# Optimization experiments

Hardware: AMD Instinct MI355X
Metric: run time of the kernel (lower is better)

The kernel has to match this reference:

```python
import jax, jax.numpy as jnp
import numpy as np

B, T, D, H = 2, 2048, 1024, 16
HD = D // H
FF = 4 * D
EPS = 1e-5


def rmsnorm(x, w):
    var = jnp.mean(jnp.square(x), axis=-1, keepdims=True)
    return x * jax.lax.rsqrt(var + EPS) * w


def setup_inputs() -> dict:
    key = jax.random.key(0)
    ks = jax.random.split(key, 17)
    sc = 0.02
    d = {}
    d["x"] = jax.random.normal(ks[0], (B, T, D), jnp.float32)
    d["x_token"] = jax.random.normal(ks[1], (B, T, D), jnp.float32)
    d["pos_emb"] = jax.random.normal(ks[2], (T, D), jnp.float32)
    d["lc_weight"] = jax.random.normal(ks[3], (1,), jnp.float32)
    d["Wq"] = jax.random.normal(ks[4], (D, D), jnp.float32) * sc  # per-head query weights stacked
    d["Wk"] = jax.random.normal(ks[5], (D, D), jnp.float32) * sc
    d["Wv"] = jax.random.normal(ks[6], (D, D), jnp.float32) * sc
    d["proj_w"] = jax.random.normal(ks[7], (D, D), jnp.float32) * sc
    d["proj_b"] = jnp.zeros((D,), jnp.float32)
    d["w1_w"] = jax.random.normal(ks[8], (FF, D), jnp.float32) * sc
    d["w1_b"] = jnp.zeros((FF,), jnp.float32)
    d["w2_w"] = jax.random.normal(ks[9], (D, FF), jnp.float32) * sc
    d["w2_b"] = jnp.zeros((D,), jnp.float32)
    d["w3_w"] = jax.random.normal(ks[10], (FF, D), jnp.float32) * sc
    d["w3_b"] = jnp.zeros((FF,), jnp.float32)
    d["norm1_w"] = jnp.ones((D,), jnp.float32)
    d["norm2_w"] = jnp.ones((D,), jnp.float32)
    return d


def reference(x, x_token, pos_emb, lc_weight, Wq, Wk, Wv, proj_w, proj_b,
              w1_w, w1_b, w2_w, w2_b, w3_w, w3_b, norm1_w, norm2_w):
    lc = jax.nn.sigmoid(lc_weight)  # scalar gate
    x_att = lc * x + (1.0 - lc) * x_token
    xn = rmsnorm(x_att, norm1_w)

    # q, v from normed gated input; k from raw positional embedding (faithful to source)
    q = (xn @ Wq.T).reshape(B, T, H, HD)
    k = (pos_emb @ Wk.T).reshape(T, H, HD)
    v = (xn @ Wv.T).reshape(B, T, H, HD)

    # NOTE: scale uses full model dim E (=D), not head_size, as in the source
    scores = jnp.einsum('bqhd,khd->bhqk', q, k) * (D ** -0.5)
    causal = jnp.tril(jnp.ones((T, T), bool))
    scores = jnp.where(causal, scores, -jnp.inf)
    p = jax.nn.softmax(scores, axis=-1)
    attn = jnp.einsum('bhqk,bkhd->bqhd', p, v).reshape(B, T, D)

    x = x + attn @ proj_w.T + proj_b

    xn2 = rmsnorm(x, norm2_w)
    h = jax.nn.silu(xn2 @ w1_w.T + w1_b) * (xn2 @ w3_w.T + w3_b)
    return x + h @ w2_w.T + w2_b
```

## Files before the change

### kernel.cpp

```cpp
#include <hip/hip_runtime.h>
#include <hip/hip_bf16.h>


typedef __hip_bfloat16 bf16;
typedef __attribute__((ext_vector_type(8))) short bf16x8;
typedef __attribute__((ext_vector_type(4))) float floatx4;

constexpr int cB = 2, cT = 2048, cD = 1024, cH = 16, cFF = 4096;
constexpr float cEPS = 1e-5f;
constexpr unsigned BF16_ONES = 0x3F803F80u;

__device__ __forceinline__ float b2f(bf16 x) { return __bfloat162float(x); }
__device__ __forceinline__ bf16  f2b(float x) { return __float2bfloat16(x); }
__device__ __forceinline__ unsigned short f2bu(float x) {
  bf16 t = __float2bfloat16(x);
  union { bf16 b; unsigned short u; } cv;
  cv.b = t;
  return cv.u;
}
__device__ __forceinline__ float loadR(const bf16* p)  { return b2f(*p); }
__device__ __forceinline__ float loadR(const float* p) { return *p; }

__device__ __forceinline__ void gload16(const bf16* g, unsigned short* l) {
  __builtin_amdgcn_global_load_lds(
      (const __attribute__((address_space(1))) void*)g,
      (__attribute__((address_space(3))) void*)l, 16, 0, 0);
}

__device__ __forceinline__ int xcd_remap1(int lin, int n) {
  return (lin & 7) * (n >> 3) + (lin >> 3);
}
__device__ __forceinline__ void xcd_remap(int& bx, int& by, int gx, int gy) {
  const int nwg = gx * gy;
  const int lin = by * gx + bx;
  const int nl  = xcd_remap1(lin, nwg);
  bx = nl % gx;
  by = nl / gx;
}

struct ConvArgs {
  const void* src[17];
  bf16* dst[17];
  int n[17];
  int sb[17];
};

__global__ __launch_bounds__(256) void convert_all_k(ConvArgs a) {
  const int bid = blockIdx.x;
  int seg = 0;
#pragma unroll
  for (int i = 1; i < 17; i++) seg = (bid >= a.sb[i]) ? i : seg;
  const int n = a.n[seg];
  const int i0 = (bid - a.sb[seg]) * 2048 + threadIdx.x * 8;
  if (i0 >= n) return;
  const bool isb = (((const unsigned*)a.src[15])[0] == BF16_ONES);
  const void* src = a.src[seg];
  bf16* dst = a.dst[seg];
  if (i0 + 8 <= n) {
    if (isb) {
      *(int4*)(dst + i0) = *(const int4*)((const bf16*)src + i0);
    } else {
      float4 f0 = *(const float4*)((const float*)src + i0);
      float4 f1 = *(const float4*)((const float*)src + i0 + 4);
      int4 ro;
      bf16* po = (bf16*)&ro;
      po[0] = f2b(f0.x); po[1] = f2b(f0.y); po[2] = f2b(f0.z); po[3] = f2b(f0.w);
      po[4] = f2b(f1.x); po[5] = f2b(f1.y); po[6] = f2b(f1.z); po[7] = f2b(f1.w);
      *(int4*)(dst + i0) = ro;
    }
  } else {
    for (int j = i0; j < n; j++)
      dst[j] = isb ? ((const bf16*)src)[j] : f2b(((const float*)src)[j]);
  }
}

template <int OUTK, typename ResT>
__device__ __forceinline__ void gemm_core64(
    const bf16* __restrict__ A, const bf16* __restrict__ W,
    const bf16* __restrict__ bias, const ResT* __restrict__ R,
    void* __restrict__ Cv,
    int N, int Kst, int kb, int klen, int m0, int n0,
    unsigned short* As, unsigned short* Bs)
{
  const int tid  = threadIdx.x;
  const int wave = tid >> 6;
  const int lane = tid & 63;
  const int l15  = lane & 15;
  const int quad = lane >> 4;
  const int wm   = (wave >> 1) * 64;
  const int wn   = (wave & 1) * 32;

  const int lr  = lane >> 2;
  const int lc8 = (lane & 3) * 8;
  const bf16* Ag0 = A + (size_t)(m0 + wave * 32 + lr) * Kst + kb + lc8;
  const bf16* Ag1 = Ag0 + (size_t)16 * Kst;
  const bf16* Bg0 = W + (size_t)(n0 + wave * 16 + lr) * Kst + kb + lc8;
  unsigned short* lA0 = &As[(wave * 32) * 32];
  unsigned short* lA1 = &As[(wave * 32 + 16) * 32];
  unsigned short* lB0 = &Bs[(wave * 16) * 32];

  floatx4 acc[4][2];
#pragma unroll
  for (int i = 0; i < 4; i++)
#pragma unroll
    for (int j = 0; j < 2; j++) acc[i][j] = (floatx4){0.f, 0.f, 0.f, 0.f};

  for (int k0 = 0; k0 < klen; k0 += 64) {
    gload16(Ag0 + k0, lA0);
    gload16(Ag1 + k0, lA1);
    gload16(Ag0 + k0 + 32, lA0 + 128 * 32);
    gload16(Ag1 + k0 + 32, lA1 + 128 * 32);
    gload16(Bg0 + k0, lB0);
    gload16(Bg0 + k0 + 32, lB0 + 64 * 32);
    __syncthreads();

    bf16x8 a[4][2], b[2][2];
#pragma unroll
    for (int t = 0; t < 4; t++)
#pragma unroll
      for (int kh = 0; kh < 2; kh++)
        a[t][kh] = *(const bf16x8*)&As[kh * 128 * 32 + (wm + t * 16 + l15) * 32 + quad * 8];
#pragma unroll
    for (int u = 0; u < 2; u++)
#pragma unroll
      for (int kh = 0; kh < 2; kh++)
        b[u][kh] = *(const bf16x8*)&Bs[kh * 64 * 32 + (wn + u * 16 + l15) * 32 + quad * 8];
#pragma unroll
    for (int tm = 0; tm < 4; tm++)
#pragma unroll
      for (int tn = 0; tn < 2; tn++)
#pragma unroll
        for (int kh = 0; kh < 2; kh++)
          acc[tm][tn] = __builtin_amdgcn_mfma_f32_16x16x32_bf16(a[tm][kh], b[tn][kh], acc[tm][tn], 0, 0, 0);
    __syncthreads();
  }

#pragma unroll
  for (int tm = 0; tm < 4; tm++) {
#pragma unroll
    for (int tn = 0; tn < 2; tn++) {
      const int row = m0 + wm + tm * 16 + quad * 4;
      const int col = n0 + wn + tn * 16 + l15;
      float bv = (OUTK != 3 && bias) ? b2f(bias[col]) : 0.f;
#pragma unroll
      for (int i = 0; i < 4; i++) {
        float val = acc[tm][tn][i] + bv;
        const size_t cidx = (size_t)(row + i) * N + col;
        if (OUTK == 3) {
          atomicAdd((float*)Cv + cidx, val);
        } else {
          if (R) val += loadR(&R[cidx]);
          if (OUTK == 0) ((bf16*)Cv)[cidx] = f2b(val);
          else           ((float*)Cv)[cidx] = val;
        }
      }
    }
  }
}

template <int OUTK, typename ResT>
__global__ __launch_bounds__(256) void gemm_f(
    const bf16* __restrict__ A, const bf16* __restrict__ W,
    const bf16* __restrict__ bias, const ResT* __restrict__ R,
    void* __restrict__ Cv, int N, int Kst, int kchunk, int gx, int gxy)
{
  __shared__ __align__(16) unsigned short As[2 * 128 * 32];
  __shared__ __align__(16) unsigned short Bs[2 * 64 * 32];
  const int lin = xcd_remap1(blockIdx.x, gridDim.x);
  const int kz  = lin / gxy;
  const int rem = lin % gxy;
  gemm_core64<OUTK, ResT>(A, W, bias, R, Cv, N, Kst, kz * kchunk, kchunk,
                          (rem / gx) * 128, (rem % gx) * 64, As, Bs);
}

__global__ __launch_bounds__(256) void gemm_qkv(
    const bf16* __restrict__ xn, const bf16* __restrict__ pos,
    const bf16* __restrict__ Wq, const bf16* __restrict__ Wv,
    const bf16* __restrict__ Wk,
    bf16* __restrict__ q, bf16* __restrict__ v, bf16* __restrict__ kb)
{
  __shared__ __align__(16) unsigned short As[2 * 128 * 32];
  __shared__ __align__(16) unsigned short Bs[2 * 64 * 32];
  const int lin = xcd_remap1(blockIdx.x, gridDim.x);
  int z, local;
  if (lin < 512)       { z = 0; local = lin; }
  else if (lin < 1024) { z = 1; local = lin - 512; }
  else                 { z = 2; local = lin - 1024; }
  const int gx = 16;
  const int by = local / gx, bx = local % gx;
  const bf16* A = (z == 2) ? pos : xn;
  const bf16* W = (z == 0) ? Wq : (z == 1) ? Wv : Wk;
  bf16* C = (z == 0) ? q : (z == 1) ? v : kb;
  gemm_core64<0, bf16>(A, W, nullptr, (const bf16*)nullptr, C,
                       cD, cD, 0, cD, by * 128, bx * 64, As, Bs);
}

__global__ __launch_bounds__(256) void gemm_w13(
    const bf16* __restrict__ A,
    const bf16* __restrict__ W1, const bf16* __restrict__ b1,
    const bf16* __restrict__ W3, const bf16* __restrict__ b3,
    bf16* __restrict__ H, int N, int K)
{
  __shared__ __align__(16) unsigned short As[2 * 128 * 32];
  __shared__ __align__(16) unsigned short B1s[2 * 64 * 32];
  __shared__ __align__(16) unsigned short B3s[2 * 64 * 32];
  const int lin = xcd_remap1(blockIdx.x, gridDim.x);
  const int by  = lin & 31;
  const int bx  = lin >> 5;
  const int m0  = by * 128;
  const int n0  = bx * 64;

  const int tid  = threadIdx.x;
  const int wave = tid >> 6;
  const int lane = tid & 63;
  const int l15  = lane & 15;
  const int quad = lane >> 4;
  const int wm   = (wave >> 1) * 64;
  const int wn   = (wave & 1) * 32;

  const int lr  = lane >> 2;
  const int lc8 = (lane & 3) * 8;
  const bf16* Ag0  = A  + (size_t)(m0 + wave * 32 + lr) * K + lc8;
  const bf16* Ag1  = Ag0 + (size_t)16 * K;
  const bf16* B1g0 = W1 + (size_t)(n0 + wave * 16 + lr) * K + lc8;
  const bf16* B3g0 = W3 + (size_t)(n0 + wave * 16 + lr) * K + lc8;
  unsigned short* lA0 = &As[(wave * 32) * 32];
  unsigned short* lA1 = &As[(wave * 32 + 16) * 32];
  unsigned short* l1B = &B1s[(wave * 16) * 32];
  unsigned short* l3B = &B3s[(wave * 16) * 32];

  floatx4 acc1[4][2], acc3[4][2];
#pragma unroll
  for (int i = 0; i < 4; i++)
#pragma unroll
    for (int j = 0; j < 2; j++) {
      acc1[i][j] = (floatx4){0.f, 0.f, 0.f, 0.f};
      acc3[i][j] = (floatx4){0.f, 0.f, 0.f, 0.f};
    }

  for (int k0 = 0; k0 < K; k0 += 64) {
    gload16(Ag0 + k0, lA0);
    gload16(Ag1 + k0, lA1);
    gload16(Ag0 + k0 + 32, lA0 + 128 * 32);
    gload16(Ag1 + k0 + 32, lA1 + 128 * 32);
    gload16(B1g0 + k0, l1B);
    gload16(B1g0 + k0 + 32, l1B + 64 * 32);
    gload16(B3g0 + k0, l3B);
    gload16(B3g0 + k0 + 32, l3B + 64 * 32);
    __syncthreads();

    bf16x8 a[4][2], v1[2][2], v3[2][2];
#pragma unroll
    for (int t = 0; t < 4; t++)
#pragma unroll
      for (int kh = 0; kh < 2; kh++)
        a[t][kh] = *(const bf16x8*)&As[kh * 128 * 32 + (wm + t * 16 + l15) * 32 + quad * 8];
#pragma unroll
    for (int u = 0; u < 2; u++)
#pragma unroll
      for (int kh = 0; kh < 2; kh++) {
        v1[u][kh] = *(const bf16x8*)&B1s[kh * 64 * 32 + (wn + u * 16 + l15) * 32 + quad * 8];
        v3[u][kh] = *(const bf16x8*)&B3s[kh * 64 * 32 + (wn + u * 16 + l15) * 32 + quad * 8];
      }
#pragma unroll
    for (int tm = 0; tm < 4; tm++)
#pragma unroll
      for (int tn = 0; tn < 2; tn++)
#pragma unroll
        for (int kh = 0; kh < 2; kh++) {
          acc1[tm][tn] = __builtin_amdgcn_mfma_f32_16x16x32_bf16(a[tm][kh], v1[tn][kh], acc1[tm][tn], 0, 0, 0);
          acc3[tm][tn] = __builtin_amdgcn_mfma_f32_16x16x32_bf16(a[tm][kh], v3[tn][kh], acc3[tm][tn], 0, 0, 0);
        }
    __syncthreads();
  }

#pragma unroll
  for (int tm = 0; tm < 4; tm++) {
#pragma unroll
    for (int tn = 0; tn < 2; tn++) {
      const int row = m0 + wm + tm * 16 + quad * 4;
      const int col = n0 + wn + tn * 16 + l15;
      const float bv1 = b2f(b1[col]);
      const float bv3 = b2f(b3[col]);
#pragma unroll
      for (int i = 0; i < 4; i++) {
        float g = acc1[tm][tn][i] + bv1;
        float u = acc3[tm][tn][i] + bv3;
        float val = g * (1.f / (1.f + __expf(-g))) * u;
        H[(size_t)(row + i) * N + col] = f2b(val);
      }
    }
  }
}

template <bool GATE, typename InT>
__global__ __launch_bounds__(256) void rmsnorm_k(
    const InT* __restrict__ X, const bf16* __restrict__ XT,
    const bf16* __restrict__ LC, const bf16* __restrict__ Wn,
    bf16* __restrict__ O, float* __restrict__ Z)
{
  const int row = blockIdx.x;
  const int tid = threadIdx.x;
  const size_t base = (size_t)row * cD;
  const int c = tid * 4;

  if (Z) *(float4*)(Z + base + c) = (float4){0.f, 0.f, 0.f, 0.f};

  float lc = 1.f, lc1 = 0.f;
  if (GATE) {
    float g = b2f(LC[0]);
    lc = 1.f / (1.f + __expf(-g));
    lc1 = 1.f - lc;
  }

  float xv[4];
  if (sizeof(InT) == 2) {
    ushort4 u = *(const ushort4*)((const unsigned short*)X + base + c);
    const bf16* pu = (const bf16*)&u;
#pragma unroll
    for (int i = 0; i < 4; i++) xv[i] = b2f(pu[i]);
  } else {
    float4 f = *(const float4*)((const float*)X + base + c);
    xv[0] = f.x; xv[1] = f.y; xv[2] = f.z; xv[3] = f.w;
  }
  if (GATE) {
    ushort4 u = *(const ushort4*)((const unsigned short*)XT + base + c);
    const bf16* pu = (const bf16*)&u;
#pragma unroll
    for (int i = 0; i < 4; i++) xv[i] = lc * xv[i] + lc1 * b2f(pu[i]);
  }

  float ss = xv[0] * xv[0] + xv[1] * xv[1] + xv[2] * xv[2] + xv[3] * xv[3];
#pragma unroll
  for (int off = 32; off; off >>= 1) ss += __shfl_xor(ss, off, 64);

  __shared__ float red[4];
  if ((tid & 63) == 0) red[tid >> 6] = ss;
  __syncthreads();
  float tot = red[0] + red[1] + red[2] + red[3];
  float rs = rsqrtf(tot * (1.f / cD) + cEPS);

  ushort4 o;
  bf16* po = (bf16*)&o;
#pragma unroll
  for (int i = 0; i < 4; i++) po[i] = f2b(xv[i] * rs * b2f(Wn[c + i]));
  *(ushort4*)((unsigned short*)O + base + c) = o;
}

__global__ __launch_bounds__(256) void combine_k(
    const float* __restrict__ P, const float* __restrict__ X2,
    const bf16* __restrict__ bias, void* __restrict__ out,
    const unsigned* __restrict__ dbits)
{
  const bool obf = (*dbits == BF16_ONES);
  const size_t idx = ((size_t)blockIdx.x * 256 + threadIdx.x) * 4;
  float4 p = *(const float4*)(P + idx);
  float4 x = *(const float4*)(X2 + idx);
  const int col = (int)(idx & (cD - 1));
  ushort4 bu = *(const ushort4*)((const unsigned short*)bias + col);
  const bf16* bb = (const bf16*)&bu;
  float v0 = p.x + x.x + b2f(bb[0]);
  float v1 = p.y + x.y + b2f(bb[1]);
  float v2 = p.z + x.z + b2f(bb[2]);
  float v3 = p.w + x.w + b2f(bb[3]);
  if (obf) {
    ushort4 o;
    bf16* po = (bf16*)&o;
    po[0] = f2b(v0); po[1] = f2b(v1); po[2] = f2b(v2); po[3] = f2b(v3);
    *(ushort4*)((unsigned short*)out + idx) = o;
  } else {
    *(float4*)((float*)out + idx) = (float4){v0, v1, v2, v3};
  }
}

__global__ __launch_bounds__(256) void fattn_k(
    const bf16* __restrict__ Q, const bf16* __restrict__ K,
    const bf16* __restrict__ V, bf16* __restrict__ O)
{
  constexpr int LQ = 72, LK = 72, LV = 72;
  __shared__ __align__(16) unsigned short Qs[64 * LQ];
  __shared__ __align__(16) unsigned short Ks[64 * LK];
  __shared__ __align__(16) unsigned short Vs[64 * LV];

  const int tid  = threadIdx.x;
  const int wave = tid >> 6;
  const int lane = tid & 63;
  const int l15  = lane & 15;
  const int quad = lane >> 4;
  const int blk  = blockIdx.x;
  const int qt   = 31 - (blk & 31);
  const int h    = (blk >> 5) & 15;
  const int b    = blk >> 9;
  const int q0   = qt * 64;

  const bf16* Qb = Q + ((size_t)b * cT) * cD + h * 64;
  const bf16* Kb = K + h * 64;
  const bf16* Vb = V + ((size_t)b * cT) * cD + h * 64;

  {
    const int qr = tid >> 2, qc = (tid & 3) * 16;
    const bf16* gq = Qb + (size_t)(q0 + qr) * cD + qc;
    *(int4*)&Qs[qr * LQ + qc]     = *(const int4*)(gq);
    *(int4*)&Qs[qr * LQ + qc + 8] = *(const int4*)(gq + 8);
  }
  __syncthreads();

  const int qw = wave * 16;
  bf16x8 qa[2];
#pragma unroll
  for (int dc = 0; dc < 2; dc++)
    qa[dc] = *(const bf16x8*)&Qs[(qw + l15) * LQ + dc * 32 + quad * 8];

  float l_p[4] = {0.f, 0.f, 0.f, 0.f};
  floatx4 oacc[4];
#pragma unroll
  for (int dt = 0; dt < 4; dt++) oacc[dt] = (floatx4){0.f, 0.f, 0.f, 0.f};

  const int ktiles = qt + 1;
  unsigned short* Pw = &Qs[qw * LQ];

  const int kr = tid >> 2, kc = (tid & 3) * 16;
  int4 kpre0, kpre1;
  unsigned short vpre[16];
  {
    const bf16* g = Kb + (size_t)kr * cD + kc;
    kpre0 = *(const int4*)g;
    kpre1 = *(const int4*)(g + 8);
    const unsigned short* gv = (const unsigned short*)(Vb + (size_t)(wave * 16) * cD + lane);
#pragma unroll
    for (int j = 0; j < 16; j++) vpre[j] = gv[(size_t)j * cD];
  }

  for (int it = 0; it < ktiles; ++it) {
    const int k0 = it * 64;
    __syncthreads();
    *(int4*)&Ks[kr * LK + kc]     = kpre0;
    *(int4*)&Ks[kr * LK + kc + 8] = kpre1;
    {
      union { unsigned short us[8]; int4 v4; } pk0, pk1;
#pragma unroll
      for (int j = 0; j < 8; j++) { pk0.us[j] = vpre[j]; pk1.us[j] = vpre[8 + j]; }
      *(int4*)&Vs[lane * LV + wave * 16]     = pk0.v4;
      *(int4*)&Vs[lane * LV + wave * 16 + 8] = pk1.v4;
    }
    __syncthreads();

    if (it + 1 < ktiles) {
      const bf16* g = Kb + (size_t)(k0 + 64 + kr) * cD + kc;
      kpre0 = *(const int4*)g;
      kpre1 = *(const int4*)(g + 8);
      const unsigned short* gv = (const unsigned short*)(Vb + (size_t)(k0 + 64 + wave * 16) * cD + lane);
#pragma unroll
      for (int j = 0; j < 16; j++) vpre[j] = gv[(size_t)j * cD];
    }

    floatx4 s[4];
#pragma unroll
    for (int st = 0; st < 4; st++) {
      bf16x8 kb0 = *(const bf16x8*)&Ks[(st * 16 + l15) * LK + quad * 8];
      bf16x8 kb1 = *(const bf16x8*)&Ks[(st * 16 + l15) * LK + 32 + quad * 8];
      s[st] = (floatx4){0.f, 0.f, 0.f, 0.f};
      s[st] = __builtin_amdgcn_mfma_f32_16x16x32_bf16(qa[0], kb0, s[st], 0, 0, 0);
      s[st] = __builtin_amdgcn_mfma_f32_16x16x32_bf16(qa[1], kb1, s[st], 0, 0, 0);
    }
    float p[4][4];
#pragma unroll
    for (int i = 0; i < 4; i++) {
      const int qrow = q0 + qw + quad * 4 + i;
#pragma unroll
      for (int st = 0; st < 4; st++) {
        const int kp = k0 + st * 16 + l15;
        float pv = (kp > qrow) ? 0.f : __expf(s[st][i] * 0.03125f);
        p[st][i] = pv;
        l_p[i] += pv;
      }
    }
#pragma unroll
    for (int st = 0; st < 4; st++)
#pragma unroll
      for (int i = 0; i < 4; i++)
        Pw[(quad * 4 + i) * LQ + st * 16 + l15] = f2bu(p[st][i]);
    bf16x8 pa[2];
#pragma unroll
    for (int pc = 0; pc < 2; pc++)
      pa[pc] = *(const bf16x8*)&Pw[l15 * LQ + pc * 32 + quad * 8];
#pragma unroll
    for (int dt = 0; dt < 4; dt++) {
      bf16x8 vb0 = *(const bf16x8*)&Vs[(dt * 16 + l15) * LV + quad * 8];
      bf16x8 vb1 = *(const bf16x8*)&Vs[(dt * 16 + l15) * LV + 32 + quad * 8];
      oacc[dt] = __builtin_amdgcn_mfma_f32_16x16x32_bf16(pa[0], vb0, oacc[dt], 0, 0, 0);
      oacc[dt] = __builtin_amdgcn_mfma_f32_16x16x32_bf16(pa[1], vb1, oacc[dt], 0, 0, 0);
    }
  }

  float rl[4];
#pragma unroll
  for (int i = 0; i < 4; i++) {
    float li = l_p[i];
#pragma unroll
    for (int off = 1; off < 16; off <<= 1) li += __shfl_xor(li, off, 64);
    rl[i] = 1.f / li;
  }
  const size_t obase = ((size_t)b * cT + q0 + qw) * cD + h * 64;
#pragma unroll
  for (int dt = 0; dt < 4; dt++)
#pragma unroll
    for (int i = 0; i < 4; i++)
      O[obase + (size_t)(quad * 4 + i) * cD + dt * 16 + l15] = f2b(oacc[dt][i] * rl[i]);
}

extern "C" void kernel_launch(void* const* d_in, const int* in_sizes, int n_in,
                              void* d_out, int out_size, void* d_ws, size_t ws_size,
                              hipStream_t stream) {
  char* ws = (char*)d_ws;
  const size_t MB = 1u << 20;
  const int BT = cB * cT;

  bf16* cxt  = (bf16*)(ws + 0);
  bf16* cpos = (bf16*)(ws + 8 * MB);
  bf16* q    = (bf16*)(ws + 12 * MB);
  bf16* kbuf = (bf16*)(ws + 20 * MB);
  bf16* v    = (bf16*)(ws + 24 * MB);
  bf16* h    = (bf16*)(ws + 0);
  size_t off = 32 * MB;
  auto alloc = [&](size_t bytes) -> char* {
    char* p = ws + off;
    off = (off + bytes + 255) & ~(size_t)255;
    return p;
  };
  bf16*  cx  = (bf16*)alloc((size_t)BT * cD * 2);
  bf16*  xn  = (bf16*)alloc((size_t)BT * cD * 2);
  float* x2  = (float*)alloc((size_t)BT * cD * 4);
  bf16*  xn2 = (bf16*)alloc((size_t)BT * cD * 2);
  float* part = (float*)(ws + 32 * MB);
  bf16* cin[17];
  cin[0] = cx; cin[1] = cxt; cin[2] = cpos;
  for (int i = 3; i < 17; i++) cin[i] = (bf16*)alloc((size_t)in_sizes[i] * 2);

  const unsigned* dbits = (const unsigned*)d_in[15];
  dim3 blk(256);

  ConvArgs ca;
  int nblk = 0;
  for (int i = 0; i < 17; i++) {
    ca.src[i] = d_in[i];
    ca.dst[i] = cin[i];
    ca.n[i] = in_sizes[i];
    ca.sb[i] = nblk;
    nblk += (in_sizes[i] + 2047) / 2048;
  }
  convert_all_k<<<nblk, blk, 0, stream>>>(ca);

  const bf16 *clc = cin[3], *cWq = cin[4], *cWk = cin[5], *cWv = cin[6];
  const bf16 *cprojw = cin[7], *cprojb = cin[8];
  const bf16 *cw1w = cin[9], *cw1b = cin[10], *cw2w = cin[11], *cw2b = cin[12];
  const bf16 *cw3w = cin[13], *cw3b = cin[14], *cn1 = cin[15], *cn2 = cin[16];

  rmsnorm_k<true, bf16><<<BT, blk, 0, stream>>>(cx, cxt, clc, cn1, xn, nullptr);
  gemm_qkv<<<1280, blk, 0, stream>>>(xn, cpos, cWq, cWv, cWk, q, v, kbuf);
  bf16* attn = xn;
  fattn_k<<<cB * cH * (cT / 64), blk, 0, stream>>>(q, kbuf, v, attn);
  gemm_f<1, bf16><<<512, blk, 0, stream>>>(
      attn, cprojw, cprojb, cx, x2, cD, cD, cD, 16, 512);
  rmsnorm_k<false, float><<<BT, blk, 0, stream>>>(
      x2, (const bf16*)nullptr, (const bf16*)nullptr, cn2, xn2, part);
  gemm_w13<<<2048, blk, 0, stream>>>(
      xn2, cw1w, cw1b, cw3w, cw3b, h, cFF, cD);
  gemm_f<3, float><<<1024, blk, 0, stream>>>(
      h, cw2w, nullptr, (const float*)nullptr, part, cD, cFF, 2048, 16, 512);
  combine_k<<<BT, blk, 0, stream>>>(part, x2, cw2b, d_out, dbits);
  (void)n_in; (void)out_size; (void)ws_size;
}
```

Before: 471.3 us.

## Double-buffer LDS tiles in GEMM kernels to overlap global loads with MFMA

Adds a second LDS buffer to the shared GEMM core and the fused W1/W3 GEMM. The next K-tile's global-to-LDS loads are issued right after the barrier, while MFMAs run on the current tile. This hides load latency behind compute and removes one barrier per K iteration. In exchange, LDS per block doubles (64KB for the W1/W3 kernel), which can lower how many blocks fit on a CU. The change also deletes an unused remap helper.

Measured after the change: 486.2 us. +3.2%, slower.

```diff
diff --git a/kernel.cpp b/kernel.cpp
--- a/kernel.cpp
+++ b/kernel.cpp
@@ -29,13 +29,6 @@
 
 __device__ __forceinline__ int xcd_remap1(int lin, int n) {
   return (lin & 7) * (n >> 3) + (lin >> 3);
-}
-__device__ __forceinline__ void xcd_remap(int& bx, int& by, int gx, int gy) {
-  const int nwg = gx * gy;
-  const int lin = by * gx + bx;
-  const int nl  = xcd_remap1(lin, nwg);
-  bx = nl % gx;
-  by = nl / gx;
 }
 
 struct ConvArgs {
@@ -95,9 +88,20 @@
   const bf16* Ag0 = A + (size_t)(m0 + wave * 32 + lr) * Kst + kb + lc8;
   const bf16* Ag1 = Ag0 + (size_t)16 * Kst;
   const bf16* Bg0 = W + (size_t)(n0 + wave * 16 + lr) * Kst + kb + lc8;
-  unsigned short* lA0 = &As[(wave * 32) * 32];
-  unsigned short* lA1 = &As[(wave * 32 + 16) * 32];
-  unsigned short* lB0 = &Bs[(wave * 16) * 32];
+  const int aoff0 = (wave * 32) * 32;
+  const int aoff1 = (wave * 32 + 16) * 32;
+  const int boff  = (wave * 16) * 32;
+
+  auto STAGE = [&](int buf, int k0) {
+    unsigned short* ab = As + buf * (2 * 128 * 32);
+    unsigned short* bb = Bs + buf * (2 * 64 * 32);
+    gload16(Ag0 + k0,      ab + aoff0);
+    gload16(Ag1 + k0,      ab + aoff1);
+    gload16(Ag0 + k0 + 32, ab + 128 * 32 + aoff0);
+    gload16(Ag1 + k0 + 32, ab + 128 * 32 + aoff1);
+    gload16(Bg0 + k0,      bb + boff);
+    gload16(Bg0 + k0 + 32, bb + 64 * 32 + boff);
+  };
 
   floatx4 acc[4][2];
 #pragma unroll
@@ -105,26 +109,25 @@
 #pragma unroll
     for (int j = 0; j < 2; j++) acc[i][j] = (floatx4){0.f, 0.f, 0.f, 0.f};
 
+  STAGE(0, 0);
+  int cur = 0;
   for (int k0 = 0; k0 < klen; k0 += 64) {
-    gload16(Ag0 + k0, lA0);
-    gload16(Ag1 + k0, lA1);
-    gload16(Ag0 + k0 + 32, lA0 + 128 * 32);
-    gload16(Ag1 + k0 + 32, lA1 + 128 * 32);
-    gload16(Bg0 + k0, lB0);
-    gload16(Bg0 + k0 + 32, lB0 + 64 * 32);
     __syncthreads();
-
+    if (k0 + 64 < klen) STAGE(cur ^ 1, k0 + 64);
+
+    const unsigned short* ab = As + cur * (2 * 128 * 32);
+    const unsigned short* bb = Bs + cur * (2 * 64 * 32);
     bf16x8 a[4][2], b[2][2];
 #pragma unroll
     for (int t = 0; t < 4; t++)
 #pragma unroll
       for (int kh = 0; kh < 2; kh++)
-        a[t][kh] = *(const bf16x8*)&As[kh * 128 * 32 + (wm + t * 16 + l15) * 32 + quad * 8];
+        a[t][kh] = *(const bf16x8*)&ab[kh * 128 * 32 + (wm + t * 16 + l15) * 32 + quad * 8];
 #pragma unroll
     for (int u = 0; u < 2; u++)
 #pragma unroll
       for (int kh = 0; kh < 2; kh++)
-        b[u][kh] = *(const bf16x8*)&Bs[kh * 64 * 32 + (wn + u * 16 + l15) * 32 + quad * 8];
+        b[u][kh] = *(const bf16x8*)&bb[kh * 64 * 32 + (wn + u * 16 + l15) * 32 + quad * 8];
 #pragma unroll
     for (int tm = 0; tm < 4; tm++)
 #pragma unroll
@@ -132,7 +135,7 @@
 #pragma unroll
         for (int kh = 0; kh < 2; kh++)
           acc[tm][tn] = __builtin_amdgcn_mfma_f32_16x16x32_bf16(a[tm][kh], b[tn][kh], acc[tm][tn], 0, 0, 0);
-    __syncthreads();
+    cur ^= 1;
   }
 
 #pragma unroll
@@ -164,8 +167,8 @@
     const bf16* __restrict__ bias, const ResT* __restrict__ R,
     void* __restrict__ Cv, int N, int Kst, int kchunk, int gx, int gxy)
 {
-  __shared__ __align__(16) unsigned short As[2 * 128 * 32];
-  __shared__ __align__(16) unsigned short Bs[2 * 64 * 32];
+  __shared__ __align__(16) unsigned short As[2 * 2 * 128 * 32];
+  __shared__ __align__(16) unsigned short Bs[2 * 2 * 64 * 32];
   const int lin = xcd_remap1(blockIdx.x, gridDim.x);
   const int kz  = lin / gxy;
   const int rem = lin % gxy;
@@ -179,8 +182,8 @@
     const bf16* __restrict__ Wk,
     bf16* __restrict__ q, bf16* __restrict__ v, bf16* __restrict__ kb)
 {
-  __shared__ __align__(16) unsigned short As[2 * 128 * 32];
-  __shared__ __align__(16) unsigned short Bs[2 * 64 * 32];
+  __shared__ __align__(16) unsigned short As[2 * 2 * 128 * 32];
+  __shared__ __align__(16) unsigned short Bs[2 * 2 * 64 * 32];
   const int lin = xcd_remap1(blockIdx.x, gridDim.x);
   int z, local;
   if (lin < 512)       { z = 0; local = lin; }
@@ -201,9 +204,9 @@
     const bf16* __restrict__ W3, const bf16* __restrict__ b3,
     bf16* __restrict__ H, int N, int K)
 {
-  __shared__ __align__(16) unsigned short As[2 * 128 * 32];
-  __shared__ __align__(16) unsigned short B1s[2 * 64 * 32];
-  __shared__ __align__(16) unsigned short B3s[2 * 64 * 32];
+  __shared__ __align__(16) unsigned short As[2 * 2 * 128 * 32];
+  __shared__ __align__(16) unsigned short B1s[2 * 2 * 64 * 32];
+  __shared__ __align__(16) unsigned short B3s[2 * 2 * 64 * 32];
   const int lin = xcd_remap1(blockIdx.x, gridDim.x);
   const int by  = lin & 31;
   const int bx  = lin >> 5;
@@ -224,10 +227,23 @@
   const bf16* Ag1  = Ag0 + (size_t)16 * K;
   const bf16* B1g0 = W1 + (size_t)(n0 + wave * 16 + lr) * K + lc8;
   const bf16* B3g0 = W3 + (size_t)(n0 + wave * 16 + lr) * K + lc8;
-  unsigned short* lA0 = &As[(wave * 32) * 32];
-  unsigned short* lA1 = &As[(wave * 32 + 16) * 32];
-  unsigned short* l1B = &B1s[(wave * 16) * 32];
-  unsigned short* l3B = &B3s[(wave * 16) * 32];
+  const int aoff0 = (wave * 32) * 32;
+  const int aoff1 = (wave * 32 + 16) * 32;
+  const int boff  = (wave * 16) * 32;
+
+  auto STAGE = [&](int buf, int k0) {
+    unsigned short* ab = As  + buf * (2 * 128 * 32);
+    unsigned short* b1b = B1s + buf * (2 * 64 * 32);
+    unsigned short* b3b = B3s + buf * (2 * 64 * 32);
+    gload16(Ag0 + k0,       ab + aoff0);
+    gload16(Ag1 + k0,       ab + aoff1);
+    gload16(Ag0 + k0 + 32,  ab + 128 * 32 + aoff0);
+    gload16(Ag1 + k0 + 32,  ab + 128 * 32 + aoff1);
+    gload16(B1g0 + k0,      b1b + boff);
+    gload16(B1g0 + k0 + 32, b1b + 64 * 32 + boff);
+    gload16(B3g0 + k0,      b3b + boff);
+    gload16(B3g0 + k0 + 32, b3b + 64 * 32 + boff);
+  };
 
   floatx4 acc1[4][2], acc3[4][2];
 #pragma unroll
@@ -238,29 +254,27 @@
       acc3[i][j] = (floatx4){0.f, 0.f, 0.f, 0.f};
     }
 
+  STAGE(0, 0);
+  int cur = 0;
   for (int k0 = 0; k0 < K; k0 += 64) {
-    gload16(Ag0 + k0, lA0);
-    gload16(Ag1 + k0, lA1);
-    gload16(Ag0 + k0 + 32, lA0 + 128 * 32);
-    gload16(Ag1 + k0 + 32, lA1 + 128 * 32);
-    gload16(B1g0 + k0, l1B);
-    gload16(B1g0 + k0 + 32, l1B + 64 * 32);
-    gload16(B3g0 + k0, l3B);
-    gload16(B3g0 + k0 + 32, l3B + 64 * 32);
     __syncthreads();
-
+    if (k0 + 64 < K) STAGE(cur ^ 1, k0 + 64);
+
+    const unsigned short* ab  = As  + cur * (2 * 128 * 32);
+    const unsigned short* b1b = B1s + cur * (2 * 64 * 32);
+    const unsigned short* b3b = B3s + cur * (2 * 64 * 32);
     bf16x8 a[4][2], v1[2][2], v3[2][2];
 #pragma unroll
     for (int t = 0; t < 4; t++)
 #pragma unroll
       for (int kh = 0; kh < 2; kh++)
-        a[t][kh] = *(const bf16x8*)&As[kh * 128 * 32 + (wm + t * 16 + l15) * 32 + quad * 8];
+        a[t][kh] = *(const bf16x8*)&ab[kh * 128 * 32 + (wm + t * 16 + l15) * 32 + quad * 8];
 #pragma unroll
     for (int u = 0; u < 2; u++)
 #pragma unroll
       for (int kh = 0; kh < 2; kh++) {
-        v1[u][kh] = *(const bf16x8*)&B1s[kh * 64 * 32 + (wn + u * 16 + l15) * 32 + quad * 8];
-        v3[u][kh] = *(const bf16x8*)&B3s[kh * 64 * 32 + (wn + u * 16 + l15) * 32 + quad * 8];
+        v1[u][kh] = *(const bf16x8*)&b1b[kh * 64 * 32 + (wn + u * 16 + l15) * 32 + quad * 8];
+        v3[u][kh] = *(const bf16x8*)&b3b[kh * 64 * 32 + (wn + u * 16 + l15) * 32 + quad * 8];
       }
 #pragma unroll
     for (int tm = 0; tm < 4; tm++)
@@ -271,7 +285,7 @@
           acc1[tm][tn] = __builtin_amdgcn_mfma_f32_16x16x32_bf16(a[tm][kh], v1[tn][kh], acc1[tm][tn], 0, 0, 0);
           acc3[tm][tn] = __builtin_amdgcn_mfma_f32_16x16x32_bf16(a[tm][kh], v3[tn][kh], acc3[tm][tn], 0, 0, 0);
         }
-    __syncthreads();
+    cur ^= 1;
   }
 
 #pragma unroll
```

## Replace fused W1/W3 GEMM with two 256x256-tile pipelined GEMMs

Applied to the files above, without the earlier changes.

The fused SwiGLU up-projection kernel (128x64 tiles, two B operands) is replaced by a templated 512-thread GEMM with 256x256 tiles, double-buffered LDS with async global-to-LDS loads, XOR-swizzled LDS layout, and s_setprio around MFMA blocks. It is launched twice: the first pass writes silu(W1 x + b1) to h, the second multiplies W3 x + b3 into h in place. The goal is higher arithmetic intensity and overlap of loads with MFMA, at the cost of an extra read/write round trip of the h buffer and an extra launch.

Measured after the change: 477.1 us. Within noise of the previous version (+1.2%).

```diff
diff --git a/kernel.cpp b/kernel.cpp
--- a/kernel.cpp
+++ b/kernel.cpp
@@ -29,13 +29,6 @@
 
 __device__ __forceinline__ int xcd_remap1(int lin, int n) {
   return (lin & 7) * (n >> 3) + (lin >> 3);
-}
-__device__ __forceinline__ void xcd_remap(int& bx, int& by, int gx, int gy) {
-  const int nwg = gx * gy;
-  const int lin = by * gx + bx;
-  const int nl  = xcd_remap1(lin, nwg);
-  bx = nl % gx;
-  by = nl / gx;
 }
 
 struct ConvArgs {
@@ -195,99 +188,151 @@
                        cD, cD, 0, cD, by * 128, bx * 64, As, Bs);
 }
 
-__global__ __launch_bounds__(256) void gemm_w13(
-    const bf16* __restrict__ A,
-    const bf16* __restrict__ W1, const bf16* __restrict__ b1,
-    const bf16* __restrict__ W3, const bf16* __restrict__ b3,
-    bf16* __restrict__ H, int N, int K)
+template <int MODE>
+__global__ __launch_bounds__(512, 2) void gemm8p(
+    const bf16* __restrict__ A, const bf16* __restrict__ W,
+    const bf16* __restrict__ bias, bf16* H)
 {
-  __shared__ __align__(16) unsigned short As[2 * 128 * 32];
-  __shared__ __align__(16) unsigned short B1s[2 * 64 * 32];
-  __shared__ __align__(16) unsigned short B3s[2 * 64 * 32];
+  __shared__ __align__(16) unsigned short As[2 * 2 * 256 * 32];
+  __shared__ __align__(16) unsigned short Bs[2 * 2 * 256 * 32];
+  constexpr int K = cD;
+  constexpr int NT = K / 64;
   const int lin = xcd_remap1(blockIdx.x, gridDim.x);
-  const int by  = lin & 31;
-  const int bx  = lin >> 5;
-  const int m0  = by * 128;
-  const int n0  = bx * 64;
+  const int by = lin >> 4, bx = lin & 15;
+  const int m0 = by * 256, n0 = bx * 256;
 
   const int tid  = threadIdx.x;
   const int wave = tid >> 6;
   const int lane = tid & 63;
   const int l15  = lane & 15;
   const int quad = lane >> 4;
-  const int wm   = (wave >> 1) * 64;
-  const int wn   = (wave & 1) * 32;
-
-  const int lr  = lane >> 2;
-  const int lc8 = (lane & 3) * 8;
-  const bf16* Ag0  = A  + (size_t)(m0 + wave * 32 + lr) * K + lc8;
-  const bf16* Ag1  = Ag0 + (size_t)16 * K;
-  const bf16* B1g0 = W1 + (size_t)(n0 + wave * 16 + lr) * K + lc8;
-  const bf16* B3g0 = W3 + (size_t)(n0 + wave * 16 + lr) * K + lc8;
-  unsigned short* lA0 = &As[(wave * 32) * 32];
-  unsigned short* lA1 = &As[(wave * 32 + 16) * 32];
-  unsigned short* l1B = &B1s[(wave * 16) * 32];
-  unsigned short* l3B = &B3s[(wave * 16) * 32];
-
-  floatx4 acc1[4][2], acc3[4][2];
-#pragma unroll
-  for (int i = 0; i < 4; i++)
-#pragma unroll
-    for (int j = 0; j < 2; j++) {
-      acc1[i][j] = (floatx4){0.f, 0.f, 0.f, 0.f};
-      acc3[i][j] = (floatx4){0.f, 0.f, 0.f, 0.f};
-    }
-
-  for (int k0 = 0; k0 < K; k0 += 64) {
-    gload16(Ag0 + k0, lA0);
-    gload16(Ag1 + k0, lA1);
-    gload16(Ag0 + k0 + 32, lA0 + 128 * 32);
-    gload16(Ag1 + k0 + 32, lA1 + 128 * 32);
-    gload16(B1g0 + k0, l1B);
-    gload16(B1g0 + k0 + 32, l1B + 64 * 32);
-    gload16(B3g0 + k0, l3B);
-    gload16(B3g0 + k0 + 32, l3B + 64 * 32);
-    __syncthreads();
-
-    bf16x8 a[4][2], v1[2][2], v3[2][2];
-#pragma unroll
-    for (int t = 0; t < 4; t++)
-#pragma unroll
-      for (int kh = 0; kh < 2; kh++)
-        a[t][kh] = *(const bf16x8*)&As[kh * 128 * 32 + (wm + t * 16 + l15) * 32 + quad * 8];
-#pragma unroll
-    for (int u = 0; u < 2; u++)
-#pragma unroll
-      for (int kh = 0; kh < 2; kh++) {
-        v1[u][kh] = *(const bf16x8*)&B1s[kh * 64 * 32 + (wn + u * 16 + l15) * 32 + quad * 8];
-        v3[u][kh] = *(const bf16x8*)&B3s[kh * 64 * 32 + (wn + u * 16 + l15) * 32 + quad * 8];
-      }
-#pragma unroll
-    for (int tm = 0; tm < 4; tm++)
-#pragma unroll
-      for (int tn = 0; tn < 2; tn++)
-#pragma unroll
-        for (int kh = 0; kh < 2; kh++) {
-          acc1[tm][tn] = __builtin_amdgcn_mfma_f32_16x16x32_bf16(a[tm][kh], v1[tn][kh], acc1[tm][tn], 0, 0, 0);
-          acc3[tm][tn] = __builtin_amdgcn_mfma_f32_16x16x32_bf16(a[tm][kh], v3[tn][kh], acc3[tm][tn], 0, 0, 0);
+  const int wm   = wave >> 2;
+  const int wq   = wave & 3;
+  const int swz  = (quad ^ (l15 & 3)) * 8;
+
+  const int srow = wave * 32 + (lane >> 2);
+  const int sblk = (lane & 3) ^ ((lane >> 2) & 3);
+  const bf16* Ags = A + (size_t)(m0 + srow) * K + sblk * 8;
+  const bf16* Wgs = W + (size_t)(n0 + srow) * K + sblk * 8;
+  unsigned short* const lA = &As[0] + (wave * 32) * 32;
+  unsigned short* const lB = &Bs[0] + (wave * 32) * 32;
+
+  floatx4 acc[8][4];
+#pragma unroll
+  for (int i = 0; i < 8; i++)
+#pragma unroll
+    for (int j = 0; j < 4; j++) acc[i][j] = (floatx4){0.f, 0.f, 0.f, 0.f};
+
+#define STAGE_A8(buf, kel, kh)                                              \
+  { const bf16* s_ = Ags + (kel) + (kh) * 32;                               \
+    unsigned short* d_ = lA + (buf) * (2 * 256 * 32) + (kh) * (256 * 32);   \
+    gload16(s_, d_);                                                        \
+    gload16(s_ + (size_t)16 * K, d_ + 16 * 32); }
+#define STAGE_B8(buf, kel, kh)                                              \
+  { const bf16* s_ = Wgs + (kel) + (kh) * 32;                               \
+    unsigned short* d_ = lB + (buf) * (2 * 256 * 32) + (kh) * (256 * 32);   \
+    gload16(s_, d_);                                                        \
+    gload16(s_ + (size_t)16 * K, d_ + 16 * 32); }
+
+#define WAITBAR4()                                                          \
+  asm volatile("s_waitcnt vmcnt(4)" ::: "memory");                          \
+  __builtin_amdgcn_sched_barrier(0);                                        \
+  __builtin_amdgcn_s_barrier();                                             \
+  __builtin_amdgcn_sched_barrier(0);
+
+  STAGE_A8(0, 0, 0); STAGE_B8(0, 0, 0); STAGE_A8(0, 0, 1); STAGE_B8(0, 0, 1);
+  asm volatile("s_waitcnt vmcnt(0)" ::: "memory");
+  __builtin_amdgcn_sched_barrier(0);
+  __builtin_amdgcn_s_barrier();
+  __builtin_amdgcn_sched_barrier(0);
+
+  int buf = 0;
+  for (int t = 0; t < NT; ++t) {
+    const int nkel = (t + 1) * 64;
+    const bool pf = (t + 1 < NT);
+    const unsigned short* ab = &As[0] + buf * (2 * 256 * 32);
+    const unsigned short* bb = &Bs[0] + buf * (2 * 256 * 32);
+    bf16x8 bfr[4], af[4];
+
+    WAITBAR4();
+    if (pf) STAGE_A8(buf ^ 1, nkel, 0);
+#pragma unroll
+    for (int nf = 0; nf < 4; nf++)
+      bfr[nf] = *(const bf16x8*)&bb[(wq * 64 + nf * 16 + l15) * 32 + swz];
+#pragma unroll
+    for (int j = 0; j < 4; j++)
+      af[j] = *(const bf16x8*)&ab[(wm * 128 + j * 16 + l15) * 32 + swz];
+    __builtin_amdgcn_s_setprio(1);
+#pragma unroll
+    for (int j = 0; j < 4; j++)
+#pragma unroll
+      for (int nf = 0; nf < 4; nf++)
+        acc[j][nf] = __builtin_amdgcn_mfma_f32_16x16x32_bf16(af[j], bfr[nf], acc[j][nf], 0, 0, 0);
+    __builtin_amdgcn_s_setprio(0);
+
+    if (pf) STAGE_B8(buf ^ 1, nkel, 0);
+#pragma unroll
+    for (int j = 0; j < 4; j++)
+      af[j] = *(const bf16x8*)&ab[(wm * 128 + 64 + j * 16 + l15) * 32 + swz];
+    __builtin_amdgcn_s_setprio(1);
+#pragma unroll
+    for (int j = 0; j < 4; j++)
+#pragma unroll
+      for (int nf = 0; nf < 4; nf++)
+        acc[4 + j][nf] = __builtin_amdgcn_mfma_f32_16x16x32_bf16(af[j], bfr[nf], acc[4 + j][nf], 0, 0, 0);
+    __builtin_amdgcn_s_setprio(0);
+
+    WAITBAR4();
+    if (pf) STAGE_A8(buf ^ 1, nkel, 1);
+#pragma unroll
+    for (int nf = 0; nf < 4; nf++)
+      bfr[nf] = *(const bf16x8*)&bb[256 * 32 + (wq * 64 + nf * 16 + l15) * 32 + swz];
+#pragma unroll
+    for (int j = 0; j < 4; j++)
+      af[j] = *(const bf16x8*)&ab[256 * 32 + (wm * 128 + j * 16 + l15) * 32 + swz];
+    __builtin_amdgcn_s_setprio(1);
+#pragma unroll
+    for (int j = 0; j < 4; j++)
+#pragma unroll
+      for (int nf = 0; nf < 4; nf++)
+        acc[j][nf] = __builtin_amdgcn_mfma_f32_16x16x32_bf16(af[j], bfr[nf], acc[j][nf], 0, 0, 0);
+    __builtin_amdgcn_s_setprio(0);
+
+    if (pf) STAGE_B8(buf ^ 1, nkel, 1);
+#pragma unroll
+    for (int j = 0; j < 4; j++)
+      af[j] = *(const bf16x8*)&ab[256 * 32 + (wm * 128 + 64 + j * 16 + l15) * 32 + swz];
+    __builtin_amdgcn_s_setprio(1);
+#pragma unroll
+    for (int j = 0; j < 4; j++)
+#pragma unroll
+      for (int nf = 0; nf < 4; nf++)
+        acc[4 + j][nf] = __builtin_amdgcn_mfma_f32_16x16x32_bf16(af[j], bfr[nf], acc[4 + j][nf], 0, 0, 0);
+    __builtin_amdgcn_s_setprio(0);
+
+    buf ^= 1;
+  }
+#undef STAGE_A8
+#undef STAGE_B8
+#undef WAITBAR4
+
+#pragma unroll
+  for (int mf = 0; mf < 8; mf++) {
+#pragma unroll
+    for (int nf = 0; nf < 4; nf++) {
+      const int row = m0 + wm * 128 + mf * 16 + quad * 4;
+      const int col = n0 + wq * 64 + nf * 16 + l15;
+      const float bv = b2f(bias[col]);
+#pragma unroll
+      for (int i = 0; i < 4; i++) {
+        const size_t idx = (size_t)(row + i) * cFF + col;
+        float v = acc[mf][nf][i] + bv;
+        if (MODE == 0) {
+          v = v * (1.f / (1.f + __expf(-v)));
+          H[idx] = f2b(v);
+        } else {
+          H[idx] = f2b(v * b2f(H[idx]));
         }
-    __syncthreads();
-  }
-
-#pragma unroll
-  for (int tm = 0; tm < 4; tm++) {
-#pragma unroll
-    for (int tn = 0; tn < 2; tn++) {
-      const int row = m0 + wm + tm * 16 + quad * 4;
-      const int col = n0 + wn + tn * 16 + l15;
-      const float bv1 = b2f(b1[col]);
-      const float bv3 = b2f(b3[col]);
-#pragma unroll
-      for (int i = 0; i < 4; i++) {
-        float g = acc1[tm][tn][i] + bv1;
-        float u = acc3[tm][tn][i] + bv3;
-        float val = g * (1.f / (1.f + __expf(-g))) * u;
-        H[(size_t)(row + i) * N + col] = f2b(val);
       }
     }
   }
@@ -564,8 +609,8 @@
       attn, cprojw, cprojb, cx, x2, cD, cD, cD, 16, 512);
   rmsnorm_k<false, float><<<BT, blk, 0, stream>>>(
       x2, (const bf16*)nullptr, (const bf16*)nullptr, cn2, xn2, part);
-  gemm_w13<<<2048, blk, 0, stream>>>(
-      xn2, cw1w, cw1b, cw3w, cw3b, h, cFF, cD);
+  gemm8p<0><<<256, 512, 0, stream>>>(xn2, cw1w, cw1b, h);
+  gemm8p<1><<<256, 512, 0, stream>>>(xn2, cw3w, cw3b, h);
   gemm_f<3, float><<<1024, blk, 0, stream>>>(
       h, cw2w, nullptr, (const float*)nullptr, part, cD, cFF, 2048, 16, 512);
   combine_k<<<BT, blk, 0, stream>>>(part, x2, cw2b, d_out, dbits);
```
